# Kernel optimization log

Measured on AMD Instinct MI355X. Metric: run time of the kernel, lower is better.

The kernel has to match this reference:

```python
import jax, jax.numpy as jnp
import numpy as np

D_MODEL = 1024
NUM_HEADS = 16
D_K = D_MODEL // NUM_HEADS
B, S = 4, 4096


def setup_inputs() -> dict:
    key = jax.random.key(0)
    ks = jax.random.split(key, 12)
    sc = 1.0 / np.sqrt(D_MODEL)
    inp = {
        "query": jax.random.normal(ks[0], (B, S, D_MODEL), dtype=jnp.float32),
        "key": jax.random.normal(ks[1], (B, S, D_MODEL), dtype=jnp.float32),
        "value": jax.random.normal(ks[2], (B, S, D_MODEL), dtype=jnp.float32),
        "w_q": jax.random.normal(ks[3], (D_MODEL, D_MODEL), dtype=jnp.float32) * sc,
        "b_q": jax.random.normal(ks[4], (D_MODEL,), dtype=jnp.float32) * sc,
        "w_k": jax.random.normal(ks[5], (D_MODEL, D_MODEL), dtype=jnp.float32) * sc,
        "b_k": jax.random.normal(ks[6], (D_MODEL,), dtype=jnp.float32) * sc,
        "w_v": jax.random.normal(ks[7], (D_MODEL, D_MODEL), dtype=jnp.float32) * sc,
        "b_v": jax.random.normal(ks[8], (D_MODEL,), dtype=jnp.float32) * sc,
        "w_o": jax.random.normal(ks[9], (D_MODEL, D_MODEL), dtype=jnp.float32) * sc,
        "b_o": jax.random.normal(ks[10], (D_MODEL,), dtype=jnp.float32) * sc,
    }
    return inp


def reference(query, key, value, w_q, b_q, w_k, b_k, w_v, b_v, w_o, b_o):
    b, s, _ = query.shape
    # projections (torch Linear: x @ W.T + b)
    Q = query @ w_q.T + b_q
    K = key @ w_k.T + b_k
    V = value @ w_v.T + b_v
    # elu+1 feature map
    Q = jax.nn.elu(Q) + 1.0
    K = jax.nn.elu(K) + 1.0
    # [b, h, s, d]
    Q = Q.reshape(b, s, NUM_HEADS, D_K).transpose(0, 2, 1, 3)
    K = K.reshape(b, s, NUM_HEADS, D_K).transpose(0, 2, 1, 3)
    V = V.reshape(b, s, NUM_HEADS, D_K).transpose(0, 2, 1, 3)
    # KV outer-sum: [b, h, d, d]
    KV = jnp.einsum("bhsd,bhse->bhde", K, V)
    Z = jnp.einsum("bhsd,bhde->bhse", Q, KV)  # [b, h, s, d]
    Ksum = K.sum(axis=-2)  # [b, h, d]
    D = jnp.einsum("bhsd,bhd->bhs", Q, Ksum)[..., None]  # [b, h, s, 1]
    Z = Z / (D + 1e-6)
    Z = Z.transpose(0, 2, 1, 3).reshape(b, s, D_MODEL)
    return Z @ w_o.T + b_o
```

## Files before the change

kernel.cpp:

```cpp
#include <hip/hip_runtime.h>
#include <stdint.h>

#define DM 1024
#define NH 16
#define DKH 64
#define BB 4
#define SS 4096
#define MM (BB*SS)

typedef __bf16 bf16x8 __attribute__((ext_vector_type(8)));
typedef float f32x4 __attribute__((ext_vector_type(4)));

__device__ __forceinline__ float bf2f(ushort u) {
  union { uint32_t i; float f; } v; v.i = ((uint32_t)u) << 16; return v.f;
}
__device__ __forceinline__ ushort f2bf(float f) {
  union { float f; uint32_t i; } v; v.f = f;
  uint32_t x = v.i;
  uint32_t r = (x + 0x7fffu + ((x >> 16) & 1u)) >> 16;
  return (ushort)r;
}
__device__ __forceinline__ void unpack8(uint4 u, float* o) {
  o[0] = bf2f((ushort)(u.x & 0xffff)); o[1] = bf2f((ushort)(u.x >> 16));
  o[2] = bf2f((ushort)(u.y & 0xffff)); o[3] = bf2f((ushort)(u.y >> 16));
  o[4] = bf2f((ushort)(u.z & 0xffff)); o[5] = bf2f((ushort)(u.z >> 16));
  o[6] = bf2f((ushort)(u.w & 0xffff)); o[7] = bf2f((ushort)(u.w >> 16));
}
__device__ __forceinline__ void unpack4(uint2 u, float* o) {
  o[0] = bf2f((ushort)(u.x & 0xffff)); o[1] = bf2f((ushort)(u.x >> 16));
  o[2] = bf2f((ushort)(u.y & 0xffff)); o[3] = bf2f((ushort)(u.y >> 16));
}

#define GLL16(g, l) __builtin_amdgcn_global_load_lds( \
    (__attribute__((address_space(1))) void*)(g), \
    (__attribute__((address_space(3))) void*)(l), 16, 0, 0)

__global__ void cast3(const float* __restrict__ s0, const float* __restrict__ s1,
                      const float* __restrict__ s2, ushort* __restrict__ d0,
                      ushort* __restrict__ d1, ushort* __restrict__ d2) {
  const int which = blockIdx.x >> 10;
  const int bid = blockIdx.x & 1023;
  const float* __restrict__ src = which == 0 ? s0 : (which == 1 ? s1 : s2);
  ushort* __restrict__ dst = which == 0 ? d0 : (which == 1 ? d1 : d2);
  const size_t NXE = (size_t)MM * DM;
  const size_t stride = (size_t)1024 * 256 * 8;
  for (size_t i = ((size_t)bid * 256 + threadIdx.x) * 8; i < NXE; i += stride) {
    float4 v0 = *reinterpret_cast<const float4*>(src + i);
    float4 v1 = *reinterpret_cast<const float4*>(src + i + 4);
    ushort tmp[8] = { f2bf(v0.x), f2bf(v0.y), f2bf(v0.z), f2bf(v0.w),
                      f2bf(v1.x), f2bf(v1.y), f2bf(v1.z), f2bf(v1.w) };
    *reinterpret_cast<uint4*>(dst + i) = *reinterpret_cast<uint4*>(tmp);
  }
}
__global__ void cast_w4(const float* __restrict__ s0, const float* __restrict__ s1,
                        const float* __restrict__ s2, const float* __restrict__ s3,
                        ushort* __restrict__ d0, ushort* __restrict__ d1,
                        ushort* __restrict__ d2, ushort* __restrict__ d3) {
  const int which = blockIdx.x >> 10;
  const int i = ((blockIdx.x & 1023) * 256 + threadIdx.x) * 4;
  const float* src = which == 0 ? s0 : (which == 1 ? s1 : (which == 2 ? s2 : s3));
  ushort* dst = which == 0 ? d0 : (which == 1 ? d1 : (which == 2 ? d2 : d3));
  float4 v = *reinterpret_cast<const float4*>(src + i);
  ushort4 o; o.x = f2bf(v.x); o.y = f2bf(v.y); o.z = f2bf(v.z); o.w = f2bf(v.w);
  *reinterpret_cast<ushort4*>(dst + i) = o;
}

template<int MODE>
__global__ __launch_bounds__(512, 2) void gemm8p(
    const ushort* __restrict__ A, const ushort* __restrict__ Bw,
    const float* __restrict__ bias, void* __restrict__ Cout) {
  constexpr int K = DM, N = DM;
  constexpr int NT = K / 32;
  __shared__ ushort smem[4][2][256 * 32];
  const int t = threadIdx.x;
  const int lane = t & 63;
  const int w = t >> 6;
  const int id = blockIdx.y * gridDim.x + blockIdx.x;
  const int cpx = (gridDim.x * gridDim.y) >> 3;
  const int swz = (id & 7) * cpx + (id >> 3);
  const int bx = swz % gridDim.x;
  const int by = swz / gridDim.x;
  const int m0 = by * 256, n0 = bx * 256;
  const int wm = w >> 2, wn = w & 3;
  const int fr = lane & 15;
  const int slot = lane >> 4;

  const int gsw = ((t & 3) ^ ((t >> 2) & 3)) * 8;
  const size_t baseA = (size_t)(m0 + (t >> 2)) * K + gsw;
  const size_t baseB = (size_t)(n0 + (t >> 2)) * K + gsw;
  const int ldsoff = w * 512;

  f32x4 acc[8][4] = {};

#define STAGE(tile) { \
    const int _b = (tile) & 3; const size_t _k = (size_t)(tile) * 32; \
    GLL16(A + baseA + _k, &smem[_b][0][ldsoff]); \
    GLL16(A + baseA + (size_t)128 * K + _k, &smem[_b][0][4096 + ldsoff]); \
    GLL16(Bw + baseB + _k, &smem[_b][1][ldsoff]); \
    GLL16(Bw + baseB + (size_t)128 * K + _k, &smem[_b][1][4096 + ldsoff]); }

  STAGE(0); STAGE(1); STAGE(2);
  asm volatile("s_waitcnt vmcnt(8)" ::: "memory");
  __builtin_amdgcn_s_barrier();
  __builtin_amdgcn_sched_barrier(0);

  for (int p = 0; p < NT; ++p) {
    const ushort* At = &smem[p & 3][0][0];
    const ushort* Bt = &smem[p & 3][1][0];
    bf16x8 bfr[4], afr[8];
#pragma unroll
    for (int ni = 0; ni < 4; ++ni) {
      const int row = wn * 64 + ni * 16 + fr;
      bfr[ni] = *reinterpret_cast<const bf16x8*>(Bt + row * 32 + ((slot ^ (fr & 3)) << 3));
    }
#pragma unroll
    for (int mi = 0; mi < 8; ++mi) {
      const int row = wm * 128 + mi * 16 + fr;
      afr[mi] = *reinterpret_cast<const bf16x8*>(At + row * 32 + ((slot ^ (fr & 3)) << 3));
    }
    if (p + 3 < NT) STAGE(p + 3);
    __builtin_amdgcn_s_setprio(1);
#pragma unroll
    for (int mi = 0; mi < 8; ++mi)
#pragma unroll
      for (int ni = 0; ni < 4; ++ni)
        acc[mi][ni] = __builtin_amdgcn_mfma_f32_16x16x32_bf16(afr[mi], bfr[ni], acc[mi][ni], 0, 0, 0);
    __builtin_amdgcn_s_setprio(0);
    if (p < NT - 1) {
      if (p < NT - 3)       asm volatile("s_waitcnt vmcnt(8)" ::: "memory");
      else if (p == NT - 3) asm volatile("s_waitcnt vmcnt(4)" ::: "memory");
      else                  asm volatile("s_waitcnt vmcnt(0)" ::: "memory");
      __builtin_amdgcn_s_barrier();
      __builtin_amdgcn_sched_barrier(0);
    }
  }
#undef STAGE

  const int fq = (lane >> 4) * 4;
  float bv[4];
#pragma unroll
  for (int ni = 0; ni < 4; ++ni) bv[ni] = bias[n0 + wn * 64 + ni * 16 + fr];
#pragma unroll
  for (int mi = 0; mi < 8; ++mi) {
#pragma unroll
    for (int ni = 0; ni < 4; ++ni) {
      const int c = n0 + wn * 64 + ni * 16 + fr;
#pragma unroll
      for (int q = 0; q < 4; ++q) {
        const int r = m0 + wm * 128 + mi * 16 + fq + q;
        float v = acc[mi][ni][q] + bv[ni];
        if constexpr (MODE == 0) v = (v > 0.f) ? (v + 1.f) : __expf(v);
        if constexpr (MODE == 2) {
          reinterpret_cast<float*>(Cout)[(size_t)r * N + c] = v;
        } else {
          reinterpret_cast<ushort*>(Cout)[(size_t)r * N + c] = f2bf(v);
        }
      }
    }
  }
}

__global__ __launch_bounds__(256) void kv_kernel(
    const ushort* __restrict__ Kp, const ushort* __restrict__ Vp,
    float* __restrict__ KVpart, float* __restrict__ Kspart) {
  __shared__ ushort KL[4][64][64];
  __shared__ ushort VL[4][64][64];
  const int bh = blockIdx.x;
  const int chunk = blockIdx.y;
  const int b = bh >> 4, h = bh & 15;
  const int t = threadIdx.x;
  const int w = t >> 6, lane = t & 63;
  const int d0 = (lane >> 2) * 4;
  const int e0 = (lane & 3) * 16;
  const int srow = lane >> 3;
  const int scol = (lane & 7) * 8;

  float acc[4][16] = {};
  float ks[4] = {};

  ushort* lk = &KL[w][0][0];
  ushort* lv = &VL[w][0][0];
  const int s_wave = chunk * 512 + w * 128;

  for (int tile = 0; tile < 2; ++tile) {
    const int s0 = s_wave + tile * 64;
    const size_t gbase = (size_t)(b * SS + s0 + srow) * DM + h * 64 + scol;
    asm volatile("s_waitcnt lgkmcnt(0)" ::: "memory");
#pragma unroll
    for (int it = 0; it < 8; ++it) {
      GLL16(Kp + gbase + (size_t)it * 8 * DM, lk + it * 512);
      GLL16(Vp + gbase + (size_t)it * 8 * DM, lv + it * 512);
    }
    asm volatile("s_waitcnt vmcnt(0)" ::: "memory");
    __builtin_amdgcn_sched_barrier(0);

#pragma unroll 2
    for (int s = 0; s < 64; ++s) {
      float kf[4], vf[16];
      uint2 uk = *reinterpret_cast<const uint2*>(&KL[w][s][d0]);
      uint4 uv0 = *reinterpret_cast<const uint4*>(&VL[w][s][e0]);
      uint4 uv1 = *reinterpret_cast<const uint4*>(&VL[w][s][e0 + 8]);
      unpack4(uk, kf);
      unpack8(uv0, vf);
      unpack8(uv1, vf + 8);
#pragma unroll
      for (int i = 0; i < 4; ++i) {
        ks[i] += kf[i];
#pragma unroll
        for (int j = 0; j < 16; ++j) acc[i][j] += kf[i] * vf[j];
      }
    }
  }

  const int slab = chunk * 4 + w;
  float* kvp = KVpart + ((size_t)slab * 64 + bh) * 4096;
#pragma unroll
  for (int i = 0; i < 4; ++i) {
#pragma unroll
    for (int j4 = 0; j4 < 4; ++j4) {
      float4 v = { acc[i][j4*4+0], acc[i][j4*4+1], acc[i][j4*4+2], acc[i][j4*4+3] };
      *reinterpret_cast<float4*>(kvp + (d0 + i) * 64 + e0 + j4 * 4) = v;
    }
  }
  if ((lane & 3) == 0) {
    float4 v = { ks[0], ks[1], ks[2], ks[3] };
    *reinterpret_cast<float4*>(Kspart + (size_t)slab * 4096 + bh * 64 + d0) = v;
  }
}

__global__ __launch_bounds__(256) void kvreduce_kernel(
    const float* __restrict__ KVpart, const float* __restrict__ Kspart,
    ushort* __restrict__ KVTx) {
  const int idx = blockIdx.x * 256 + threadIdx.x;
  const int bh = idx >> 12;
  const int d = (idx >> 6) & 63;
  const int e = idx & 63;
  float s = 0.f;
#pragma unroll
  for (int c = 0; c < 32; ++c) s += KVpart[(size_t)c * (64 * 4096) + idx];
  KVTx[(size_t)bh * 5120 + e * 64 + d] = f2bf(s);
  if (idx < 64 * 64) {
    float s2 = 0.f;
#pragma unroll
    for (int c = 0; c < 32; ++c) s2 += Kspart[(size_t)c * 4096 + idx];
    KVTx[(size_t)(idx >> 6) * 5120 + 4096 + (idx & 63)] = f2bf(s2);
  }
}

__global__ __launch_bounds__(256) void z_mfma_kernel(
    const ushort* __restrict__ Qp, const ushort* __restrict__ KVTx,
    ushort* __restrict__ Zn) {
  const int bh = blockIdx.y;
  const int b = bh >> 4, h = bh & 15;
  const int t = threadIdx.x;
  const int w = t >> 6, lane = t & 63;
  const int fr = lane & 15;
  const int kq = (lane >> 4) * 8;
  const int s0 = blockIdx.x * 128 + w * 32;

  const ushort* kvb = KVTx + (size_t)bh * 5120;
  bf16x8 bfrag[5][2];
#pragma unroll
  for (int ni = 0; ni < 5; ++ni)
#pragma unroll
    for (int ks = 0; ks < 2; ++ks)
      bfrag[ni][ks] = *reinterpret_cast<const bf16x8*>(kvb + (ni * 16 + fr) * 64 + ks * 32 + kq);

  f32x4 acc[2][5] = {};
  const size_t arow = (size_t)(b * SS + s0 + fr) * DM + h * 64;
#pragma unroll
  for (int mi = 0; mi < 2; ++mi) {
#pragma unroll
    for (int ks = 0; ks < 2; ++ks) {
      bf16x8 a = *reinterpret_cast<const bf16x8*>(Qp + arow + (size_t)mi * 16 * DM + ks * 32 + kq);
#pragma unroll
      for (int ni = 0; ni < 5; ++ni)
        acc[mi][ni] = __builtin_amdgcn_mfma_f32_16x16x32_bf16(a, bfrag[ni][ks], acc[mi][ni], 0, 0, 0);
    }
  }

#pragma unroll
  for (int mi = 0; mi < 2; ++mi) {
#pragma unroll
    for (int q = 0; q < 4; ++q) {
      const float dv = __shfl(acc[mi][4][q], lane & 48);
      const float inv = 1.f / (dv + 1e-6f);
      const int r = s0 + mi * 16 + (lane >> 4) * 4 + q;
      ushort* orow = Zn + (size_t)(b * SS + r) * DM + h * 64;
#pragma unroll
      for (int ni = 0; ni < 4; ++ni)
        orow[ni * 16 + fr] = f2bf(acc[mi][ni][q] * inv);
    }
  }
}

extern "C" void kernel_launch(void* const* d_in, const int* in_sizes, int n_in,
                              void* d_out, int out_size, void* d_ws, size_t ws_size,
                              hipStream_t stream) {
  const float* query = (const float*)d_in[0];
  const float* key_  = (const float*)d_in[1];
  const float* value = (const float*)d_in[2];
  const float* w_q = (const float*)d_in[3];
  const float* b_q = (const float*)d_in[4];
  const float* w_k = (const float*)d_in[5];
  const float* b_k = (const float*)d_in[6];
  const float* w_v = (const float*)d_in[7];
  const float* b_v = (const float*)d_in[8];
  const float* w_o = (const float*)d_in[9];
  const float* b_o = (const float*)d_in[10];

  char* ws = (char*)d_ws;
  const size_t NX = (size_t)MM * DM;
  ushort* Xq = (ushort*)ws; ws += NX * 2;
  ushort* Xk = (ushort*)ws; ws += NX * 2;
  ushort* Xv = (ushort*)ws; ws += NX * 2;
  ushort* Wq = (ushort*)ws; ws += (size_t)DM * DM * 2;
  ushort* Wk = (ushort*)ws; ws += (size_t)DM * DM * 2;
  ushort* Wv = (ushort*)ws; ws += (size_t)DM * DM * 2;
  ushort* Wo = (ushort*)ws; ws += (size_t)DM * DM * 2;
  ushort* Qp = (ushort*)ws; ws += NX * 2;
  ushort* Kp = (ushort*)ws; ws += NX * 2;
  ushort* Vp = (ushort*)ws; ws += NX * 2;
  ushort* KVTx = (ushort*)ws; ws += (size_t)64 * 80 * 64 * 2;
  ushort* Zn = (ushort*)ws; ws += NX * 2;

  float* KVpart = (float*)Xq;
  float* Kspart = (float*)Xk;

  cast3<<<3 * 1024, 256, 0, stream>>>(query, key_, value, Xq, Xk, Xv);
  cast_w4<<<4 * 1024, 256, 0, stream>>>(w_q, w_k, w_v, w_o, Wq, Wk, Wv, Wo);

  dim3 gg(DM / 256, MM / 256);
  gemm8p<0><<<gg, 512, 0, stream>>>(Xq, Wq, b_q, Qp);
  gemm8p<0><<<gg, 512, 0, stream>>>(Xk, Wk, b_k, Kp);
  gemm8p<1><<<gg, 512, 0, stream>>>(Xv, Wv, b_v, Vp);

  kv_kernel<<<dim3(64, 8), 256, 0, stream>>>(Kp, Vp, KVpart, Kspart);
  hipMemsetAsync(KVTx, 0, (size_t)64 * 80 * 64 * 2, stream);
  kvreduce_kernel<<<1024, 256, 0, stream>>>(KVpart, Kspart, KVTx);
  z_mfma_kernel<<<dim3(32, 64), 256, 0, stream>>>(Qp, KVTx, Zn);

  gemm8p<2><<<gg, 512, 0, stream>>>(Zn, Wo, b_o, d_out);
}
```

Measured before the change: 294.0 us.

## Fuse fp32-to-bf16 input cast into projection GEMM A-tile loads

Removes the separate cast3 pass over query/key/value and has a new GEMM variant read fp32 activations directly, converting them to bf16 in registers before writing swizzled A tiles into LDS. B tiles still use direct global-to-LDS loads. This cuts one full read and write of the three large activation tensors. In exchange, A loads now go through registers with manual waitcnt pipelining, which doubles A global traffic per tile and adds register pressure. KV partial buffers get their own workspace instead of reusing the cast buffers.

```diff
diff --git a/kernel.cpp b/kernel.cpp
--- a/kernel.cpp
+++ b/kernel.cpp
@@ -30,28 +30,18 @@
   o[0] = bf2f((ushort)(u.x & 0xffff)); o[1] = bf2f((ushort)(u.x >> 16));
   o[2] = bf2f((ushort)(u.y & 0xffff)); o[3] = bf2f((ushort)(u.y >> 16));
 }
+__device__ __forceinline__ uint4 pack8(uint4 lo, uint4 hi) {
+  const float* f0 = (const float*)&lo;
+  const float* f1 = (const float*)&hi;
+  ushort o[8] = { f2bf(f0[0]), f2bf(f0[1]), f2bf(f0[2]), f2bf(f0[3]),
+                  f2bf(f1[0]), f2bf(f1[1]), f2bf(f1[2]), f2bf(f1[3]) };
+  return *reinterpret_cast<uint4*>(o);
+}
 
 #define GLL16(g, l) __builtin_amdgcn_global_load_lds( \
     (__attribute__((address_space(1))) void*)(g), \
     (__attribute__((address_space(3))) void*)(l), 16, 0, 0)
 
-__global__ void cast3(const float* __restrict__ s0, const float* __restrict__ s1,
-                      const float* __restrict__ s2, ushort* __restrict__ d0,
-                      ushort* __restrict__ d1, ushort* __restrict__ d2) {
-  const int which = blockIdx.x >> 10;
-  const int bid = blockIdx.x & 1023;
-  const float* __restrict__ src = which == 0 ? s0 : (which == 1 ? s1 : s2);
-  ushort* __restrict__ dst = which == 0 ? d0 : (which == 1 ? d1 : d2);
-  const size_t NXE = (size_t)MM * DM;
-  const size_t stride = (size_t)1024 * 256 * 8;
-  for (size_t i = ((size_t)bid * 256 + threadIdx.x) * 8; i < NXE; i += stride) {
-    float4 v0 = *reinterpret_cast<const float4*>(src + i);
-    float4 v1 = *reinterpret_cast<const float4*>(src + i + 4);
-    ushort tmp[8] = { f2bf(v0.x), f2bf(v0.y), f2bf(v0.z), f2bf(v0.w),
-                      f2bf(v1.x), f2bf(v1.y), f2bf(v1.z), f2bf(v1.w) };
-    *reinterpret_cast<uint4*>(dst + i) = *reinterpret_cast<uint4*>(tmp);
-  }
-}
 __global__ void cast_w4(const float* __restrict__ s0, const float* __restrict__ s1,
                         const float* __restrict__ s2, const float* __restrict__ s3,
                         ushort* __restrict__ d0, ushort* __restrict__ d1,
@@ -160,6 +150,123 @@
   }
 }
 
+template<int MODE>
+__global__ __launch_bounds__(512, 2) void gemm8pf(
+    const float* __restrict__ A32, const ushort* __restrict__ Bw,
+    const float* __restrict__ bias, ushort* __restrict__ Cout) {
+  constexpr int K = DM, N = DM;
+  constexpr int NT = K / 32;
+  __shared__ ushort smem[4][2][256 * 32];
+  const int t = threadIdx.x;
+  const int lane = t & 63;
+  const int w = t >> 6;
+  const int id = blockIdx.y * gridDim.x + blockIdx.x;
+  const int cpx = (gridDim.x * gridDim.y) >> 3;
+  const int swz = (id & 7) * cpx + (id >> 3);
+  const int bx = swz % gridDim.x;
+  const int by = swz / gridDim.x;
+  const int m0 = by * 256, n0 = bx * 256;
+  const int wm = w >> 2, wn = w & 3;
+  const int fr = lane & 15;
+  const int slot = lane >> 4;
+
+  const int gsw = ((t & 3) ^ ((t >> 2) & 3)) * 8;
+  const size_t baseB = (size_t)(n0 + (t >> 2)) * K + gsw;
+  const int ldsoff = w * 512;
+  const int rowA = t >> 2;
+  const size_t baseA = (size_t)(m0 + rowA) * K + (t & 3) * 8;
+  const int wrs = ((t & 3) ^ (rowA & 3)) * 8;
+
+  f32x4 acc[8][4] = {};
+  uint4 SA[4], SB[4];
+
+#define STAGEB(tile) { \
+    const int _b = (tile) & 3; const size_t _k = (size_t)(tile) * 32; \
+    GLL16(Bw + baseB + _k, &smem[_b][1][ldsoff]); \
+    GLL16(Bw + baseB + (size_t)128 * K + _k, &smem[_b][1][4096 + ldsoff]); }
+#define AISSUE(tile, S) { \
+    const float* _p0 = A32 + baseA + (size_t)(tile) * 32; \
+    const float* _p1 = _p0 + (size_t)128 * K; \
+    S[0] = *reinterpret_cast<const uint4*>(_p0); \
+    S[1] = *reinterpret_cast<const uint4*>(_p0 + 4); \
+    S[2] = *reinterpret_cast<const uint4*>(_p1); \
+    S[3] = *reinterpret_cast<const uint4*>(_p1 + 4); }
+#define AWRITE(tile, S) { \
+    const int _b = (tile) & 3; \
+    *reinterpret_cast<uint4*>(&smem[_b][0][rowA * 32 + wrs]) = pack8(S[0], S[1]); \
+    *reinterpret_cast<uint4*>(&smem[_b][0][rowA * 32 + 4096 + wrs]) = pack8(S[2], S[3]); }
+
+  AISSUE(0, SA); AISSUE(1, SB);
+  STAGEB(0); STAGEB(1); STAGEB(2);
+  asm volatile("s_waitcnt vmcnt(10)" ::: "memory");
+  AWRITE(0, SA);
+  asm volatile("s_waitcnt vmcnt(4)" ::: "memory");
+  asm volatile("s_waitcnt lgkmcnt(0)" ::: "memory");
+  __builtin_amdgcn_s_barrier();
+  __builtin_amdgcn_sched_barrier(0);
+
+#define PHASE(p, IS, CS) { \
+    const ushort* At = &smem[(p) & 3][0][0]; \
+    const ushort* Bt = &smem[(p) & 3][1][0]; \
+    bf16x8 bfr[4], afr[8]; \
+    _Pragma("unroll") \
+    for (int ni = 0; ni < 4; ++ni) { \
+      const int row = wn * 64 + ni * 16 + fr; \
+      bfr[ni] = *reinterpret_cast<const bf16x8*>(Bt + row * 32 + ((slot ^ (fr & 3)) << 3)); \
+    } \
+    _Pragma("unroll") \
+    for (int mi = 0; mi < 8; ++mi) { \
+      const int row = wm * 128 + mi * 16 + fr; \
+      afr[mi] = *reinterpret_cast<const bf16x8*>(At + row * 32 + ((slot ^ (fr & 3)) << 3)); \
+    } \
+    if ((p) + 2 < NT) AISSUE((p) + 2, IS); \
+    if ((p) + 3 < NT) STAGEB((p) + 3); \
+    __builtin_amdgcn_s_setprio(1); \
+    _Pragma("unroll") \
+    for (int mi = 0; mi < 8; ++mi) \
+      _Pragma("unroll") \
+      for (int ni = 0; ni < 4; ++ni) \
+        acc[mi][ni] = __builtin_amdgcn_mfma_f32_16x16x32_bf16(afr[mi], bfr[ni], acc[mi][ni], 0, 0, 0); \
+    __builtin_amdgcn_s_setprio(0); \
+    if ((p) < NT - 1) { \
+      if ((p) < NT - 3)       asm volatile("s_waitcnt vmcnt(8)" ::: "memory"); \
+      else if ((p) == NT - 3) asm volatile("s_waitcnt vmcnt(6)" ::: "memory"); \
+      else                    asm volatile("s_waitcnt vmcnt(0)" ::: "memory"); \
+      AWRITE((p) + 1, CS); \
+      asm volatile("s_waitcnt lgkmcnt(0)" ::: "memory"); \
+      __builtin_amdgcn_s_barrier(); \
+      __builtin_amdgcn_sched_barrier(0); \
+    } }
+
+  for (int pp = 0; pp < NT; pp += 2) {
+    PHASE(pp, SA, SB);
+    PHASE(pp + 1, SB, SA);
+  }
+#undef PHASE
+#undef AWRITE
+#undef AISSUE
+#undef STAGEB
+
+  const int fq = (lane >> 4) * 4;
+  float bv[4];
+#pragma unroll
+  for (int ni = 0; ni < 4; ++ni) bv[ni] = bias[n0 + wn * 64 + ni * 16 + fr];
+#pragma unroll
+  for (int mi = 0; mi < 8; ++mi) {
+#pragma unroll
+    for (int ni = 0; ni < 4; ++ni) {
+      const int c = n0 + wn * 64 + ni * 16 + fr;
+#pragma unroll
+      for (int q = 0; q < 4; ++q) {
+        const int r = m0 + wm * 128 + mi * 16 + fq + q;
+        float v = acc[mi][ni][q] + bv[ni];
+        if constexpr (MODE == 0) v = (v > 0.f) ? (v + 1.f) : __expf(v);
+        Cout[(size_t)r * N + c] = f2bf(v);
+      }
+    }
+  }
+}
+
 __global__ __launch_bounds__(256) void kv_kernel(
     const ushort* __restrict__ Kp, const ushort* __restrict__ Vp,
     float* __restrict__ KVpart, float* __restrict__ Kspart) {
@@ -311,9 +418,6 @@
 
   char* ws = (char*)d_ws;
   const size_t NX = (size_t)MM * DM;
-  ushort* Xq = (ushort*)ws; ws += NX * 2;
-  ushort* Xk = (ushort*)ws; ws += NX * 2;
-  ushort* Xv = (ushort*)ws; ws += NX * 2;
   ushort* Wq = (ushort*)ws; ws += (size_t)DM * DM * 2;
   ushort* Wk = (ushort*)ws; ws += (size_t)DM * DM * 2;
   ushort* Wv = (ushort*)ws; ws += (size_t)DM * DM * 2;
@@ -321,19 +425,17 @@
   ushort* Qp = (ushort*)ws; ws += NX * 2;
   ushort* Kp = (ushort*)ws; ws += NX * 2;
   ushort* Vp = (ushort*)ws; ws += NX * 2;
+  float*  KVpart = (float*)ws; ws += (size_t)32 * 64 * 4096 * 4;
+  float*  Kspart = (float*)ws; ws += (size_t)32 * 4096 * 4;
   ushort* KVTx = (ushort*)ws; ws += (size_t)64 * 80 * 64 * 2;
   ushort* Zn = (ushort*)ws; ws += NX * 2;
 
-  float* KVpart = (float*)Xq;
-  float* Kspart = (float*)Xk;
-
-  cast3<<<3 * 1024, 256, 0, stream>>>(query, key_, value, Xq, Xk, Xv);
   cast_w4<<<4 * 1024, 256, 0, stream>>>(w_q, w_k, w_v, w_o, Wq, Wk, Wv, Wo);
 
   dim3 gg(DM / 256, MM / 256);
-  gemm8p<0><<<gg, 512, 0, stream>>>(Xq, Wq, b_q, Qp);
-  gemm8p<0><<<gg, 512, 0, stream>>>(Xk, Wk, b_k, Kp);
-  gemm8p<1><<<gg, 512, 0, stream>>>(Xv, Wv, b_v, Vp);
+  gemm8pf<0><<<gg, 512, 0, stream>>>(query, Wq, b_q, Qp);
+  gemm8pf<0><<<gg, 512, 0, stream>>>(key_,  Wk, b_k, Kp);
+  gemm8pf<1><<<gg, 512, 0, stream>>>(value, Wv, b_v, Vp);
 
   kv_kernel<<<dim3(64, 8), 256, 0, stream>>>(Kp, Vp, KVpart, Kspart);
   hipMemsetAsync(KVTx, 0, (size_t)64 * 80 * 64 * 2, stream);
```

New measurement: 311.9 us. 6.1% more time.
